# Kernel optimization log

Measured on AMD Instinct MI355X. Metric: run time of the kernel, lower is better.

## Reference

```python
import jax, jax.numpy as jnp
import numpy as np

B, T, S, F_IN, F_OUT, K, L = 8, 8, 500, 32, 64, 3, 3


def setup_inputs() -> dict:
    key = jax.random.key(0)
    ks = jax.random.split(key, 10)
    x = jax.random.normal(ks[0], (B, T, S, F_IN), dtype=jnp.float32)
    Adj_t = jax.random.uniform(ks[1], (T, T), dtype=jnp.float32)
    Adj_s = jax.random.uniform(ks[2], (S, S), dtype=jnp.float32)
    # small mixing coefficients so Adj^k stays numerically tame
    s = jax.random.uniform(ks[3], (4,), dtype=jnp.float32) * 0.005
    H = jax.random.normal(ks[4], (L, K, F_OUT, F_OUT), dtype=jnp.float32) / jnp.sqrt(F_OUT)
    W1 = jax.random.normal(ks[5], (F_OUT, F_IN), dtype=jnp.float32) / jnp.sqrt(F_IN)
    b1 = jax.random.normal(ks[6], (F_OUT,), dtype=jnp.float32) * 0.01
    W2 = jax.random.normal(ks[7], (F_OUT, F_OUT), dtype=jnp.float32) / jnp.sqrt(F_OUT)
    b2 = jax.random.normal(ks[8], (F_OUT,), dtype=jnp.float32) * 0.01
    merge = jax.random.normal(ks[9], (T,), dtype=jnp.float32)
    return {"x": x, "Adj_t": Adj_t, "Adj_s": Adj_s, "s": s, "H": H,
            "W1": W1, "b1": b1, "W2": W2, "b2": b2, "merge": merge}


def reference(x, Adj_t, Adj_s, s, H, W1, b1, W2, b2, merge):
    Bx, Tx, Sx, Fin = x.shape
    N = Tx * Sx
    n_layers, Kk = H.shape[0], H.shape[1]
    I_t = jnp.eye(Tx, dtype=x.dtype)
    I_s = jnp.eye(Sx, dtype=x.dtype)
    I_st = jnp.eye(N, dtype=x.dtype)
    # mixed Kronecker product-graph adjacency, (T*S) x (T*S)
    Adj = (s[0] * I_st
           + s[1] * jnp.kron(I_t, Adj_s)
           + s[2] * jnp.kron(Adj_t, I_s)
           + s[3] * jnp.kron(Adj_t, Adj_s))
    # cache Adj^k for k = 0..K-1 (same math as per-layer matrix_power)
    powers = [I_st]
    for _ in range(1, Kk):
        powers.append(powers[-1] @ Adj)
    xf = x.reshape(Bx, N, Fin) @ W1.T + b1  # [B, N, F_out]
    for l in range(n_layers):
        acc = jnp.zeros_like(xf)
        for k in range(Kk):
            acc = acc + jnp.einsum('nm,bmf->bnf', powers[k], xf) @ H[l, k]
        xf = jnp.tanh(acc)
    xf = xf @ W2.T + b2  # [B, N, F_out]
    xo = xf.reshape(Bx, Tx, Sx, -1)  # [B, T, S, F_out]
    # transpose(3,1) -> [B,F,S,T]; matmul(merge) contracts T; transpose(2,1) -> [B,S,F]
    return jnp.einsum('btsf,t->bsf', xo, merge)
```

## Files before the change

kernel.cpp:

```cpp
#include <hip/hip_runtime.h>

#define BB 8
#define TT 8
#define SS 500
#define SP 512
#define FIN 32
#define FF 64
#define NBT 64
#define KT 1536
#define LROW_S 136
#define LROW_T 264

typedef short bf16x8 __attribute__((ext_vector_type(8)));
typedef float floatx4 __attribute__((ext_vector_type(4)));

__device__ __forceinline__ unsigned f2bf(float x) {
    unsigned u = __builtin_bit_cast(unsigned, x);
    return (u + 0x7FFFu + ((u >> 16) & 1u)) >> 16;
}
__device__ __forceinline__ float bf2f(unsigned short h) {
    unsigned u = ((unsigned)h) << 16;
    return __builtin_bit_cast(float, u);
}

__device__ __forceinline__ void ctab(int m, float s0, float s1, float s2, float s3,
                                     float& c0, float& c1, float& c2) {
    c0 = 0.f; c1 = 0.f; c2 = 0.f;
    switch (m) {
        case 0: c0 = 1.f; c1 = s0; c2 = s0 * s0; break;
        case 1: c1 = s1; c2 = 2.f * s0 * s1; break;
        case 2: c2 = s1 * s1; break;
        case 3: c1 = s2; c2 = 2.f * s0 * s2; break;
        case 4: c1 = s3; c2 = 2.f * (s0 * s3 + s1 * s2); break;
        case 5: c2 = 2.f * s1 * s3; break;
        case 6: c2 = s2 * s2; break;
        case 7: c2 = 2.f * s2 * s3; break;
        case 8: c2 = s3 * s3; break;
    }
}

__global__ __launch_bounds__(256) void setup_k(const float* __restrict__ x,
                                               const float* __restrict__ W1,
                                               const float* __restrict__ b1,
                                               const float* __restrict__ As,
                                               const float* __restrict__ At,
                                               const float* __restrict__ sc,
                                               const float* __restrict__ H,
                                               unsigned short* __restrict__ Asb,
                                               unsigned short* __restrict__ AsbT,
                                               unsigned short* __restrict__ GbigT,
                                               unsigned short* __restrict__ xfT,
                                               unsigned short* __restrict__ Abig0) {
    int tid = threadIdx.x;
    if (blockIdx.x < 512) {
        __shared__ float Xs[64][FIN + 1];
        __shared__ float Wl[FIN][FF];
        __shared__ float Ot[64][FF + 1];
        __shared__ float bl[FF];
        int bt = blockIdx.x >> 3, s0 = (blockIdx.x & 7) * 64;
        int b = bt >> 3, t = bt & 7;

        for (int i = tid; i < FIN * FF; i += 256) { int f = i >> 5, j = i & 31; Wl[j][f] = W1[i]; }
        if (tid < FF) bl[tid] = b1[tid];
        const float* xb = x + (size_t)bt * SS * FIN;
        #pragma unroll
        for (int i = 0; i < 8; ++i) {
            int lin = i * 256 + tid; int r = lin >> 5, j = lin & 31;
            int s = s0 + r;
            Xs[r][j] = (s < SS) ? xb[(size_t)s * FIN + j] : 0.f;
        }
        __syncthreads();
        int f = tid & 63, sq = tid >> 6;
        for (int i = 0; i < 16; ++i) {
            int r = sq * 16 + i;
            float acc = bl[f];
            #pragma unroll
            for (int j = 0; j < FIN; ++j) acc += Xs[r][j] * Wl[j][f];
            Ot[r][f] = (s0 + r < SS) ? acc : 0.f;
        }
        __syncthreads();
        #pragma unroll
        for (int it = 0; it < 2; ++it) {
            int idx = it * 256 + tid;
            int row = idx >> 3, c = idx & 7;
            int4 w;
            unsigned short tmp[8];
            #pragma unroll
            for (int q = 0; q < 8; ++q) tmp[q] = (unsigned short)f2bf(Ot[row][c * 8 + q]);
            w.x = tmp[0] | (tmp[1] << 16); w.y = tmp[2] | (tmp[3] << 16);
            w.z = tmp[4] | (tmp[5] << 16); w.w = tmp[6] | (tmp[7] << 16);
            *(int4*)(Abig0 + (size_t)(b * SP + s0 + row) * KT + t * 192 + c * 8) = w;
        }
        {
            int ff = tid >> 2, scol = (tid & 3) * 16;
            unsigned short tmp[16];
            #pragma unroll
            for (int i = 0; i < 16; ++i) tmp[i] = (unsigned short)f2bf(Ot[scol + i][ff]);
            unsigned short* dp = xfT + ((size_t)bt * FF + ff) * SP + s0 + scol;
            #pragma unroll
            for (int q = 0; q < 2; ++q) {
                int4 w;
                w.x = tmp[q*8+0] | (tmp[q*8+1] << 16); w.y = tmp[q*8+2] | (tmp[q*8+3] << 16);
                w.z = tmp[q*8+4] | (tmp[q*8+5] << 16); w.w = tmp[q*8+6] | (tmp[q*8+7] << 16);
                *(int4*)(dp + q * 8) = w;
            }
        }
        return;
    }
    int idx = (blockIdx.x - 512) * 256 + tid;
    if (idx < 262144) {
        int s = idx >> 9, k = idx & 511;
        Asb[idx] = (s < SS && k < SS) ? (unsigned short)f2bf(As[(size_t)s * SS + k]) : 0;
    } else if (idx < 524288) {
        int r = idx - 262144;
        int j = r >> 9, k = r & 511;
        AsbT[r] = (j < SS && k < SS) ? (unsigned short)f2bf(As[(size_t)k * SS + j]) : 0;
    } else {
        int r = idx - 524288;
        if (r < 2359296) {
            int l = r / 786432;
            int r2 = r - l * 786432;
            int t = r2 / 98304;
            int r3 = r2 - t * 98304;
            int f = r3 / 1536;
            int k = r3 - f * 1536;
            int seg = k >> 6, j = k & 63;
            int tp = seg / 3, bp = seg - tp * 3;

            float s0 = sc[0], s1 = sc[1], s2 = sc[2], s3 = sc[3];
            float w0 = (t == tp) ? 1.f : 0.f;
            float w1 = At[t * 8 + tp];
            float w2 = 0.f;
            #pragma unroll
            for (int kk = 0; kk < 8; ++kk) w2 += At[t * 8 + kk] * At[kk * 8 + tp];

            float a0, a1, a2, b0, b1, b2, d0, d1, d2;
            ctab(0 * 3 + bp, s0, s1, s2, s3, a0, a1, a2);
            ctab(1 * 3 + bp, s0, s1, s2, s3, b0, b1, b2);
            ctab(2 * 3 + bp, s0, s1, s2, s3, d0, d1, d2);
            float k0c = w0 * a0 + w1 * b0 + w2 * d0;
            float k1c = w0 * a1 + w1 * b1 + w2 * d1;
            float k2c = w0 * a2 + w1 * b2 + w2 * d2;

            float val = k0c * H[((size_t)(l * 3 + 0) * 64 + j) * 64 + f]
                      + k1c * H[((size_t)(l * 3 + 1) * 64 + j) * 64 + f]
                      + k2c * H[((size_t)(l * 3 + 2) * 64 + j) * 64 + f];
            GbigT[r] = (unsigned short)f2bf(val);
        }
    }
}

__global__ __launch_bounds__(256) void prep2_k(const unsigned short* __restrict__ Asb,
                                               const unsigned short* __restrict__ AsbT,
                                               unsigned short* __restrict__ Asqb) {
    int tid = threadIdx.x;
    int wave = tid >> 6, lane = tid & 63;
    int l16 = lane & 15, quad = lane >> 4;
    int st = blockIdx.x, ct = blockIdx.y;

    const unsigned short* ap = Asb + (size_t)(st * 16 + l16) * SP + quad * 8;
    const unsigned short* bp = AsbT + (size_t)(ct * 64 + wave * 16 + l16) * SP + quad * 8;
    floatx4 acc = {};
    #pragma unroll 4
    for (int k0 = 0; k0 < SP; k0 += 32)
        acc = __builtin_amdgcn_mfma_f32_16x16x32_bf16(*(const bf16x8*)(ap + k0),
                                                      *(const bf16x8*)(bp + k0), acc, 0, 0, 0);
    int j = ct * 64 + wave * 16 + l16;
    int i0 = st * 16 + quad * 4;
    #pragma unroll
    for (int r = 0; r < 4; ++r)
        Asqb[(size_t)(i0 + r) * SP + j] = (unsigned short)f2bf(acc[r]);
}

__global__ __launch_bounds__(256) void smm_k(const unsigned short* __restrict__ Asb,
                                             const unsigned short* __restrict__ Asqb,
                                             const unsigned short* __restrict__ xfT,
                                             unsigned short* __restrict__ Abig) {
    __shared__ unsigned short A1[64 * LROW_S];
    __shared__ unsigned short A2[64 * LROW_S];
    __shared__ unsigned short Bt[64 * LROW_S];

    int tid = threadIdx.x;
    int wave = tid >> 6, lane = tid & 63;
    int l16 = lane & 15, quad = lane >> 4;
    int m0 = blockIdx.x * 64, bt = blockIdx.y;
    int b = bt >> 3, t = bt & 7;

    const unsigned short* a1g = Asb + (size_t)m0 * SP;
    const unsigned short* a2g = Asqb + (size_t)m0 * SP;
    const unsigned short* bg  = xfT + (size_t)bt * FF * SP;

    floatx4 acc1[4] = {}, acc2[4] = {};

    for (int k0 = 0; k0 < SP; k0 += 128) {
        __syncthreads();
        #pragma unroll
        for (int it = 0; it < 4; ++it) {
            int idx = it * 256 + tid;
            int row = idx >> 4, c = idx & 15;
            int4 v1 = *(const int4*)(a1g + (size_t)row * SP + k0 + c * 8);
            int4 v2 = *(const int4*)(a2g + (size_t)row * SP + k0 + c * 8);
            int4 vb = *(const int4*)(bg  + (size_t)row * SP + k0 + c * 8);
            *(int4*)&A1[row * LROW_S + c * 8] = v1;
            *(int4*)&A2[row * LROW_S + c * 8] = v2;
            *(int4*)&Bt[row * LROW_S + c * 8] = vb;
        }
        __syncthreads();
        #pragma unroll
        for (int ks = 0; ks < 4; ++ks) {
            bf16x8 af1 = *(const bf16x8*)&A1[(wave * 16 + l16) * LROW_S + ks * 32 + quad * 8];
            bf16x8 af2 = *(const bf16x8*)&A2[(wave * 16 + l16) * LROW_S + ks * 32 + quad * 8];
            #pragma unroll
            for (int nt = 0; nt < 4; ++nt) {
                bf16x8 bf = *(const bf16x8*)&Bt[(nt * 16 + l16) * LROW_S + ks * 32 + quad * 8];
                acc1[nt] = __builtin_amdgcn_mfma_f32_16x16x32_bf16(af1, bf, acc1[nt], 0, 0, 0);
                acc2[nt] = __builtin_amdgcn_mfma_f32_16x16x32_bf16(af2, bf, acc2[nt], 0, 0, 0);
            }
        }
    }

    __syncthreads();
    #pragma unroll
    for (int nt = 0; nt < 4; ++nt)
        #pragma unroll
        for (int r = 0; r < 4; ++r) {
            A1[(wave * 16 + quad * 4 + r) * LROW_S + nt * 16 + l16] = (unsigned short)f2bf(acc1[nt][r]);
            A2[(wave * 16 + quad * 4 + r) * LROW_S + nt * 16 + l16] = (unsigned short)f2bf(acc2[nt][r]);
        }
    __syncthreads();
    int row = wave * 16 + (lane >> 2);
    int c2 = (lane & 3) * 2;
    #pragma unroll
    for (int q = 0; q < 2; ++q) {
        int c = c2 + q;
        int4 v1 = *(const int4*)&A1[row * LROW_S + c * 8];
        int4 v2 = *(const int4*)&A2[row * LROW_S + c * 8];
        size_t base = (size_t)(b * SP + m0 + row) * KT + t * 192;
        *(int4*)(Abig + base + 64 + c * 8)  = v1;
        *(int4*)(Abig + base + 128 + c * 8) = v2;
    }
}

__global__ __launch_bounds__(256) void tmix_k(const unsigned short* __restrict__ Abig,
                                              const unsigned short* __restrict__ GbigT_l,
                                              unsigned short* __restrict__ xfT_out,
                                              unsigned short* __restrict__ Abig_out) {
    __shared__ unsigned short At_[64 * LROW_T];
    __shared__ unsigned short Bt_[64 * LROW_T];

    int tid = threadIdx.x;
    int wave = tid >> 6, lane = tid & 63;
    int l16 = lane & 15, quad = lane >> 4;
    int m0 = blockIdx.x * 64, t = blockIdx.y;
    int b = m0 >> 9, s0 = m0 & 511;

    const unsigned short* ag = Abig + (size_t)m0 * KT;
    const unsigned short* bg = GbigT_l + (size_t)t * FF * KT;

    floatx4 acc[4] = {};

    for (int kk = 0; kk < 6; ++kk) {
        __syncthreads();
        #pragma unroll
        for (int it = 0; it < 8; ++it) {
            int idx = it * 256 + tid;
            int row = idx >> 5, c = idx & 31;
            int4 va = *(const int4*)(ag + (size_t)row * KT + kk * 256 + c * 8);
            int4 vb = *(const int4*)(bg + (size_t)row * KT + kk * 256 + c * 8);
            *(int4*)&At_[row * LROW_T + c * 8] = va;
            *(int4*)&Bt_[row * LROW_T + c * 8] = vb;
        }
        __syncthreads();
        #pragma unroll
        for (int ks = 0; ks < 8; ++ks) {
            bf16x8 af = *(const bf16x8*)&At_[(wave * 16 + l16) * LROW_T + ks * 32 + quad * 8];
            #pragma unroll
            for (int nt = 0; nt < 4; ++nt) {
                bf16x8 bf = *(const bf16x8*)&Bt_[(nt * 16 + l16) * LROW_T + ks * 32 + quad * 8];
                acc[nt] = __builtin_amdgcn_mfma_f32_16x16x32_bf16(af, bf, acc[nt], 0, 0, 0);
            }
        }
    }

    #pragma unroll
    for (int nt = 0; nt < 4; ++nt)
        #pragma unroll
        for (int r = 0; r < 4; ++r) acc[nt][r] = tanhf(acc[nt][r]);

    int bt = b * 8 + t;

    {
        int sbase = s0 + wave * 16 + quad * 4;
        #pragma unroll
        for (int nt = 0; nt < 4; ++nt) {
            int f = nt * 16 + l16;
            int2 w;
            w.x = (int)(f2bf(acc[nt][0]) | (f2bf(acc[nt][1]) << 16));
            w.y = (int)(f2bf(acc[nt][2]) | (f2bf(acc[nt][3]) << 16));
            *(int2*)(xfT_out + ((size_t)bt * FF + f) * SP + sbase) = w;
        }
    }

    __syncthreads();
    #pragma unroll
    for (int nt = 0; nt < 4; ++nt)
        #pragma unroll
        for (int r = 0; r < 4; ++r)
            At_[(wave * 16 + quad * 4 + r) * LROW_T + nt * 16 + l16] = (unsigned short)f2bf(acc[nt][r]);
    __syncthreads();
    {
        int row = wave * 16 + (lane >> 2);
        int c2 = (lane & 3) * 2;
        #pragma unroll
        for (int q = 0; q < 2; ++q) {
            int c = c2 + q;
            int4 v = *(const int4*)&At_[row * LROW_T + c * 8];
            *(int4*)(Abig_out + (size_t)(m0 + row) * KT + t * 192 + c * 8) = v;
        }
    }
}

__global__ __launch_bounds__(256) void zredlin2_k(const unsigned short* __restrict__ Abig,
                                                  const float* __restrict__ W2,
                                                  const float* __restrict__ b2,
                                                  const float* __restrict__ merge,
                                                  float* __restrict__ out) {
    __shared__ float Wl[FF][FF + 1];
    __shared__ float zt[16][FF + 1];
    __shared__ float ml[TT];
    int tid = threadIdx.x;
    int b = blockIdx.y, s0 = blockIdx.x * 16;

    for (int i = tid; i < FF * FF; i += 256) { int f = i >> 6, j = i & 63; Wl[j][f] = W2[i]; }
    if (tid < TT) ml[tid] = merge[tid];
    __syncthreads();

    float m[TT];
    #pragma unroll
    for (int t = 0; t < TT; ++t) m[t] = ml[t];
    float msum = 0.f;
    #pragma unroll
    for (int t = 0; t < TT; ++t) msum += m[t];

    #pragma unroll
    for (int p = 0; p < 4; ++p) {
        int lin = p * 256 + tid;
        int sl = lin >> 6, f = lin & 63;
        int s = s0 + sl;
        float acc = 0.f;
        if (s < SS) {
            #pragma unroll
            for (int t = 0; t < TT; ++t)
                acc += m[t] * bf2f(Abig[(size_t)(b * SP + s) * KT + t * 192 + f]);
        }
        zt[sl][f] = acc;
    }
    __syncthreads();

    int f = tid & 63, sq = tid >> 6;
    #pragma unroll
    for (int i = 0; i < 4; ++i) {
        int sl = sq * 4 + i;
        int s = s0 + sl;
        if (s < SS) {
            float acc = b2[f] * msum;
            #pragma unroll
            for (int j = 0; j < FF; ++j) acc += zt[sl][j] * Wl[j][f];
            out[((size_t)b * SS + s) * FF + f] = acc;
        }
    }
}

extern "C" void kernel_launch(void* const* d_in, const int* in_sizes, int n_in,
                              void* d_out, int out_size, void* d_ws, size_t ws_size,
                              hipStream_t stream) {
    const float* x     = (const float*)d_in[0];
    const float* At    = (const float*)d_in[1];
    const float* As    = (const float*)d_in[2];
    const float* sc    = (const float*)d_in[3];
    const float* H     = (const float*)d_in[4];
    const float* W1    = (const float*)d_in[5];
    const float* b1    = (const float*)d_in[6];
    const float* W2    = (const float*)d_in[7];
    const float* b2    = (const float*)d_in[8];
    const float* merge = (const float*)d_in[9];
    float* out = (float*)d_out;

    char* ws = (char*)d_ws;
    unsigned short* Asb   = (unsigned short*)(ws + 0);
    unsigned short* AsbT  = (unsigned short*)(ws + 524288);
    unsigned short* Asqb  = (unsigned short*)(ws + 1048576);
    unsigned short* GbigT = (unsigned short*)(ws + 1572864);
    unsigned short* xfT0  = (unsigned short*)(ws + 6291456);
    unsigned short* xfT1  = (unsigned short*)(ws + 10485760);
    unsigned short* Abig0 = (unsigned short*)(ws + 14680064);
    unsigned short* Abig1 = (unsigned short*)(ws + 27262976);

    setup_k<<<11776, 256, 0, stream>>>(x, W1, b1, As, At, sc, H,
                                       Asb, AsbT, GbigT, xfT0, Abig0);
    prep2_k<<<dim3(32, 8), 256, 0, stream>>>(Asb, AsbT, Asqb);

    unsigned short* xfT_cur = xfT0;  unsigned short* xfT_nxt = xfT1;
    unsigned short* Abig_cur = Abig0; unsigned short* Abig_nxt = Abig1;
    for (int l = 0; l < 3; ++l) {
        smm_k<<<dim3(8, NBT), 256, 0, stream>>>(Asb, Asqb, xfT_cur, Abig_cur);
        tmix_k<<<dim3(64, 8), 256, 0, stream>>>(Abig_cur,
                                                GbigT + (size_t)l * 8 * FF * KT,
                                                xfT_nxt, Abig_nxt);
        unsigned short* tt = xfT_cur;  xfT_cur = xfT_nxt;  xfT_nxt = tt;
        unsigned short* tb = Abig_cur; Abig_cur = Abig_nxt; Abig_nxt = tb;
    }
    zredlin2_k<<<dim3(32, 8), 256, 0, stream>>>(Abig_cur, W2, b2, merge, out);
}
```

Measured before the change: 195.9 us.

## Fuse adjacency-squared GEMM into setup kernel and skip last-layer xfT write

Computes As·As directly inside the setup kernel from the fp32 adjacency with an LDS-tiled MFMA loop. This removes the separate prep2 launch and the transposed bf16 copy of As it depended on. It also adds a flag so the final tmix layer skips writing xfT, which nothing reads afterwards. The costs are redundant global loads of As per tile in the setup blocks and a strided, scalar transposed store into LDS.

```diff
diff --git a/kernel.cpp b/kernel.cpp
--- a/kernel.cpp
+++ b/kernel.cpp
@@ -47,7 +47,7 @@
                                                const float* __restrict__ sc,
                                                const float* __restrict__ H,
                                                unsigned short* __restrict__ Asb,
-                                               unsigned short* __restrict__ AsbT,
+                                               unsigned short* __restrict__ Asqb,
                                                unsigned short* __restrict__ GbigT,
                                                unsigned short* __restrict__ xfT,
                                                unsigned short* __restrict__ Abig0) {
@@ -107,16 +107,70 @@
         }
         return;
     }
-    int idx = (blockIdx.x - 512) * 256 + tid;
+    if (blockIdx.x < 768) {
+        __shared__ unsigned short Al[16 * 72];
+        __shared__ unsigned short Bl[64 * 72];
+        int tile = blockIdx.x - 512;
+        int i0 = (tile >> 3) * 16, j0 = (tile & 7) * 64;
+        int wave = tid >> 6, lane = tid & 63;
+        int l16 = lane & 15, quad = lane >> 4;
+
+        floatx4 acc = {};
+        for (int k0 = 0; k0 < SP; k0 += 64) {
+            __syncthreads();
+            {
+                int r = tid >> 4, c4 = (tid & 15) * 4;
+                int gi = i0 + r, gk = k0 + c4;
+                float a0 = 0.f, a1 = 0.f, a2 = 0.f, a3 = 0.f;
+                if (gi < SS) {
+                    const float* p = As + (size_t)gi * SS + gk;
+                    if (gk + 0 < SS) a0 = p[0];
+                    if (gk + 1 < SS) a1 = p[1];
+                    if (gk + 2 < SS) a2 = p[2];
+                    if (gk + 3 < SS) a3 = p[3];
+                }
+                int2 w;
+                w.x = (int)(f2bf(a0) | (f2bf(a1) << 16));
+                w.y = (int)(f2bf(a2) | (f2bf(a3) << 16));
+                *(int2*)&Al[r * 72 + c4] = w;
+            }
+            {
+                int r = tid >> 2, cg = (tid & 3) * 16;
+                int gk = k0 + r;
+                float vals[16];
+                if (gk < SS) {
+                    const float* p = As + (size_t)gk * SS + j0 + cg;
+                    #pragma unroll
+                    for (int q = 0; q < 16; ++q)
+                        vals[q] = (j0 + cg + q < SS) ? p[q] : 0.f;
+                } else {
+                    #pragma unroll
+                    for (int q = 0; q < 16; ++q) vals[q] = 0.f;
+                }
+                #pragma unroll
+                for (int q = 0; q < 16; ++q)
+                    Bl[(cg + q) * 72 + r] = (unsigned short)f2bf(vals[q]);
+            }
+            __syncthreads();
+            #pragma unroll
+            for (int ks = 0; ks < 2; ++ks) {
+                bf16x8 af = *(const bf16x8*)&Al[l16 * 72 + ks * 32 + quad * 8];
+                bf16x8 bf = *(const bf16x8*)&Bl[(wave * 16 + l16) * 72 + ks * 32 + quad * 8];
+                acc = __builtin_amdgcn_mfma_f32_16x16x32_bf16(af, bf, acc, 0, 0, 0);
+            }
+        }
+        #pragma unroll
+        for (int r = 0; r < 4; ++r)
+            Asqb[(size_t)(i0 + quad * 4 + r) * SP + j0 + wave * 16 + l16] =
+                (unsigned short)f2bf(acc[r]);
+        return;
+    }
+    int idx = (blockIdx.x - 768) * 256 + tid;
     if (idx < 262144) {
         int s = idx >> 9, k = idx & 511;
         Asb[idx] = (s < SS && k < SS) ? (unsigned short)f2bf(As[(size_t)s * SS + k]) : 0;
-    } else if (idx < 524288) {
+    } else {
         int r = idx - 262144;
-        int j = r >> 9, k = r & 511;
-        AsbT[r] = (j < SS && k < SS) ? (unsigned short)f2bf(As[(size_t)k * SS + j]) : 0;
-    } else {
-        int r = idx - 524288;
         if (r < 2359296) {
             int l = r / 786432;
             int r2 = r - l * 786432;
@@ -150,28 +204,6 @@
     }
 }
 
-__global__ __launch_bounds__(256) void prep2_k(const unsigned short* __restrict__ Asb,
-                                               const unsigned short* __restrict__ AsbT,
-                                               unsigned short* __restrict__ Asqb) {
-    int tid = threadIdx.x;
-    int wave = tid >> 6, lane = tid & 63;
-    int l16 = lane & 15, quad = lane >> 4;
-    int st = blockIdx.x, ct = blockIdx.y;
-
-    const unsigned short* ap = Asb + (size_t)(st * 16 + l16) * SP + quad * 8;
-    const unsigned short* bp = AsbT + (size_t)(ct * 64 + wave * 16 + l16) * SP + quad * 8;
-    floatx4 acc = {};
-    #pragma unroll 4
-    for (int k0 = 0; k0 < SP; k0 += 32)
-        acc = __builtin_amdgcn_mfma_f32_16x16x32_bf16(*(const bf16x8*)(ap + k0),
-                                                      *(const bf16x8*)(bp + k0), acc, 0, 0, 0);
-    int j = ct * 64 + wave * 16 + l16;
-    int i0 = st * 16 + quad * 4;
-    #pragma unroll
-    for (int r = 0; r < 4; ++r)
-        Asqb[(size_t)(i0 + r) * SP + j] = (unsigned short)f2bf(acc[r]);
-}
-
 __global__ __launch_bounds__(256) void smm_k(const unsigned short* __restrict__ Asb,
                                              const unsigned short* __restrict__ Asqb,
                                              const unsigned short* __restrict__ xfT,
@@ -244,7 +276,8 @@
 __global__ __launch_bounds__(256) void tmix_k(const unsigned short* __restrict__ Abig,
                                               const unsigned short* __restrict__ GbigT_l,
                                               unsigned short* __restrict__ xfT_out,
-                                              unsigned short* __restrict__ Abig_out) {
+                                              unsigned short* __restrict__ Abig_out,
+                                              int wflag) {
     __shared__ unsigned short At_[64 * LROW_T];
     __shared__ unsigned short Bt_[64 * LROW_T];
 
@@ -289,7 +322,7 @@
 
     int bt = b * 8 + t;
 
-    {
+    if (wflag) {
         int sbase = s0 + wave * 16 + quad * 4;
         #pragma unroll
         for (int nt = 0; nt < 4; ++nt) {
@@ -388,7 +421,6 @@
 
     char* ws = (char*)d_ws;
     unsigned short* Asb   = (unsigned short*)(ws + 0);
-    unsigned short* AsbT  = (unsigned short*)(ws + 524288);
     unsigned short* Asqb  = (unsigned short*)(ws + 1048576);
     unsigned short* GbigT = (unsigned short*)(ws + 1572864);
     unsigned short* xfT0  = (unsigned short*)(ws + 6291456);
@@ -396,9 +428,8 @@
     unsigned short* Abig0 = (unsigned short*)(ws + 14680064);
     unsigned short* Abig1 = (unsigned short*)(ws + 27262976);
 
-    setup_k<<<11776, 256, 0, stream>>>(x, W1, b1, As, At, sc, H,
-                                       Asb, AsbT, GbigT, xfT0, Abig0);
-    prep2_k<<<dim3(32, 8), 256, 0, stream>>>(Asb, AsbT, Asqb);
+    setup_k<<<11008, 256, 0, stream>>>(x, W1, b1, As, At, sc, H,
+                                       Asb, Asqb, GbigT, xfT0, Abig0);
 
     unsigned short* xfT_cur = xfT0;  unsigned short* xfT_nxt = xfT1;
     unsigned short* Abig_cur = Abig0; unsigned short* Abig_nxt = Abig1;
@@ -406,7 +437,7 @@
         smm_k<<<dim3(8, NBT), 256, 0, stream>>>(Asb, Asqb, xfT_cur, Abig_cur);
         tmix_k<<<dim3(64, 8), 256, 0, stream>>>(Abig_cur,
                                                 GbigT + (size_t)l * 8 * FF * KT,
-                                                xfT_nxt, Abig_nxt);
+                                                xfT_nxt, Abig_nxt, (l < 2) ? 1 : 0);
         unsigned short* tt = xfT_cur;  xfT_cur = xfT_nxt;  xfT_nxt = tt;
         unsigned short* tb = Abig_cur; Abig_cur = Abig_nxt; Abig_nxt = tb;
     }
```

After: 201.3 us. 2.8% more time.
